# Kernel optimization log

Measured on AMD Instinct MI355X. Metric: run time of the kernel, lower is better.

The kernel has to match this reference:

```python
import jax, jax.numpy as jnp
import numpy as np

N = 50000
E = 640000
R = 8


def setup_inputs() -> dict:
    key = jax.random.key(0)
    ks = jax.random.split(key, 12)
    in_c, hid_c, out_c = 128, 128, 64
    s1 = 1.0 / np.sqrt(in_c)
    s2 = 1.0 / np.sqrt(hid_c)
    s3 = 1.0 / np.sqrt(out_c)
    return {
        "x": jax.random.normal(ks[0], (N, in_c), dtype=jnp.float32),
        "edge_index": jax.random.randint(ks[1], (2, E), 0, N),
        "edge_type": jax.random.randint(ks[2], (E,), 0, R),
        # layer 1: per-relation weights, root weight, bias
        "W1": jax.random.uniform(ks[3], (R, in_c, hid_c), minval=-s1, maxval=s1, dtype=jnp.float32),
        "root1": jax.random.uniform(ks[4], (in_c, hid_c), minval=-s1, maxval=s1, dtype=jnp.float32),
        "b1": jnp.zeros((hid_c,), dtype=jnp.float32),
        # layer 2
        "W2": jax.random.uniform(ks[5], (R, hid_c, out_c), minval=-s2, maxval=s2, dtype=jnp.float32),
        "root2": jax.random.uniform(ks[6], (hid_c, out_c), minval=-s2, maxval=s2, dtype=jnp.float32),
        "b2": jnp.zeros((out_c,), dtype=jnp.float32),
        # classifier
        "Wc": jax.random.uniform(ks[7], (out_c, 2), minval=-s3, maxval=s3, dtype=jnp.float32),
        "bc": jnp.zeros((2,), dtype=jnp.float32),
    }


def _rgcn_layer(x, edge_index, edge_type, W, root, b):
    # PyG RGCNConv with aggr='mean': per relation r, mean-aggregate source
    # features over edges of type r into destinations, then apply W_r.
    # out = sum_r mean_agg_r(x) @ W_r + x @ root + b
    src, dst = edge_index[0], edge_index[1]
    msgs = x[src]  # [E, Fin] gather
    seg = edge_type * N + dst  # combined (relation, dst) segment id
    sums = jax.ops.segment_sum(msgs, seg, num_segments=R * N)  # [R*N, Fin]
    cnt = jax.ops.segment_sum(jnp.ones((msgs.shape[0],), x.dtype), seg, num_segments=R * N)
    mean = sums / jnp.maximum(cnt, 1.0)[:, None]  # zero-degree -> 0
    mean = mean.reshape(R, N, x.shape[1])  # [R, N, Fin]
    out = jnp.einsum("rnf,rfo->no", mean, W) + x @ root + b
    return out


def reference(x, edge_index, edge_type, W1, root1, b1, W2, root2, b2, Wc, bc):
    h = jax.nn.relu(_rgcn_layer(x, edge_index, edge_type, W1, root1, b1))
    # dropout (p=0.3) is identity in eval mode
    h = jax.nn.relu(_rgcn_layer(h, edge_index, edge_type, W2, root2, b2))
    logits = h @ Wc + bc  # [N, 2]
    return logits
```

## Files before the change

### kernel.cpp

```cpp
#include <hip/hip_runtime.h>

#define NN 50000
#define EE 640000
#define RR 8
#define CAP 64

typedef __bf16 bf16x8 __attribute__((ext_vector_type(8)));
typedef float  f32x4  __attribute__((ext_vector_type(4)));
typedef const __attribute__((address_space(1))) unsigned int* gas_p;
typedef __attribute__((address_space(3))) unsigned int* las_p;

__device__ __forceinline__ unsigned short f2b(float f) {
  unsigned int u = __float_as_uint(f);
  u += 0x7fffu + ((u >> 16) & 1u);
  return (unsigned short)(u >> 16);
}
__device__ __forceinline__ float b2f(unsigned short h) {
  return __uint_as_float(((unsigned int)h) << 16);
}

__global__ void k_f32_to_bf16_x4(const float* __restrict__ src,
                                 unsigned short* __restrict__ dst, int n4) {
  int t = blockIdx.x * blockDim.x + threadIdx.x;
  if (t >= n4) return;
  float4 v = reinterpret_cast<const float4*>(src)[t];
  ushort4 o = make_ushort4(f2b(v.x), f2b(v.y), f2b(v.z), f2b(v.w));
  reinterpret_cast<ushort4*>(dst)[t] = o;
}

__global__ void k_build_b1(const float* __restrict__ W1, const float* __restrict__ root1,
                           unsigned short* __restrict__ B1T) {
  int t = blockIdx.x * 256 + threadIdx.x;
  if (t >= 1152 * 128) return;
  int j = t >> 7, k = t & 127;
  float v = (j < 1024) ? W1[((j >> 7) << 14) + (k << 7) + (j & 127)]
                       : root1[(k << 7) + (j - 1024)];
  B1T[t] = f2b(v);
}

__global__ void k_build_b2(const float* __restrict__ W2, const float* __restrict__ root2,
                           unsigned short* __restrict__ B2T) {
  int t = blockIdx.x * 256 + threadIdx.x;
  if (t >= 640 * 128) return;
  int j = t >> 7, k = t & 127;
  float v = 0.0f;
  if (j < 512)      v = W2[((j >> 6) << 13) + (k << 6) + (j & 63)];
  else if (j < 576) v = root2[(k << 6) + (j - 512)];
  B2T[t] = f2b(v);
}

__global__ void k_edges(const int* __restrict__ src, const int* __restrict__ dst,
                        const int* __restrict__ typ,
                        int* __restrict__ cursor, unsigned int* __restrict__ entries) {
  int e = blockIdx.x * 256 + threadIdx.x;
  if (e >= EE) return;
  int d = dst[e], r = typ[e];
  int pos = atomicAdd(&cursor[d], 1);
  if (pos < CAP)
    entries[d * CAP + pos] = (unsigned int)src[e] | ((unsigned int)r << 16);
}

__global__ __launch_bounds__(256, 2) void k_gemm(
    const unsigned short* __restrict__ A, const unsigned short* __restrict__ BT,
    unsigned short* __restrict__ Y, float* __restrict__ rootOut,
    const float* __restrict__ bias, int M, int nsplit, int nroot, int nsub) {
  __shared__ __align__(16) unsigned short As[128 * 128];
  __shared__ __align__(16) unsigned short Bs[2][64 * 128];
  const int tid = threadIdx.x;
  const int m0 = blockIdx.x * 128;
  const int n0g = blockIdx.y * nsub * 64;

  {
#pragma unroll
    for (int c = 0; c < 8; ++c) {
      int L = tid + c * 256;
      int r = L >> 4, c16 = L & 15;
      int j = c16 ^ (r & 15);
      __builtin_amdgcn_global_load_lds(
          (gas_p)(const void*)(A + (size_t)(m0 + r) * 128 + j * 8),
          (las_p)(void*)(As + r * 128 + c16 * 8), 16, 0, 0);
    }
    const unsigned short* Gb = BT + (size_t)n0g * 128;
#pragma unroll
    for (int c = 0; c < 4; ++c) {
      int L = tid + c * 256;
      int r = L >> 4, c16 = L & 15;
      int j = c16 ^ (r & 15);
      __builtin_amdgcn_global_load_lds(
          (gas_p)(const void*)(Gb + (size_t)r * 128 + j * 8),
          (las_p)(void*)(Bs[0] + r * 128 + c16 * 8), 16, 0, 0);
    }
  }
  __syncthreads();

  const int lane = tid & 63;
  const int wave = tid >> 6;
  const int wm = (wave >> 1) << 6;
  const int wn = (wave & 1) << 5;
  const int l15 = lane & 15;
  const int quad = lane >> 4;

  const int tr = lane >> 2;
  const int tc = lane & 3;
  const int sl0 = ((tc & 1) << 1) * 16 + tr;
  const int sl1 = sl0 + 16;
  const bool thi = (tc & 2) != 0;

  int buf = 0;
  for (int s = 0; s < nsub; ++s) {
    if (s + 1 < nsub) {
      const unsigned short* Gb = BT + (size_t)(n0g + (s + 1) * 64) * 128;
      unsigned short* Lb = Bs[buf ^ 1];
#pragma unroll
      for (int c = 0; c < 4; ++c) {
        int L = tid + c * 256;
        int r = L >> 4, c16 = L & 15;
        int j = c16 ^ (r & 15);
        __builtin_amdgcn_global_load_lds(
            (gas_p)(const void*)(Gb + (size_t)r * 128 + j * 8),
            (las_p)(void*)(Lb + r * 128 + c16 * 8), 16, 0, 0);
      }
    }

    f32x4 acc[4][2] = {};
    const unsigned short* Bc = Bs[buf];
#pragma unroll
    for (int kk = 0; kk < 4; ++kk) {
      const int sw = ((kk * 4 + quad) ^ l15) * 8;
      bf16x8 af[4], bfr[2];
#pragma unroll
      for (int i = 0; i < 4; ++i)
        af[i] = *reinterpret_cast<const bf16x8*>(&As[(wm + i * 16 + l15) * 128 + sw]);
#pragma unroll
      for (int j = 0; j < 2; ++j)
        bfr[j] = *reinterpret_cast<const bf16x8*>(&Bc[(wn + j * 16 + l15) * 128 + sw]);
#pragma unroll
      for (int i = 0; i < 4; ++i)
#pragma unroll
        for (int j = 0; j < 2; ++j)
          acc[i][j] = __builtin_amdgcn_mfma_f32_16x16x32_bf16(bfr[j], af[i], acc[i][j], 0, 0, 0);
    }
    __syncthreads();

    const int scol = n0g + s * 64;
    if (scol >= nsplit) {
#pragma unroll
      for (int i = 0; i < 4; ++i) {
        const int m = wm + i * 16 + l15;
        if (m0 + m >= M) continue;
#pragma unroll
        for (int j = 0; j < 2; ++j) {
          const int col = scol + wn + j * 16 + quad * 4 - nsplit;
          if (col < nroot) {
            float4 b4 = *reinterpret_cast<const float4*>(&bias[col]);
            float4 v = make_float4(acc[i][j][0] + b4.x, acc[i][j][1] + b4.y,
                                   acc[i][j][2] + b4.z, acc[i][j][3] + b4.w);
            *reinterpret_cast<float4*>(&rootOut[(size_t)(m0 + m) * nroot + col]) = v;
          }
        }
      }
    } else {
#pragma unroll
      for (int i = 0; i < 4; ++i) {
        uint2 pk0, pk1;
        pk0.x = (unsigned int)f2b(acc[i][0][0]) | ((unsigned int)f2b(acc[i][0][1]) << 16);
        pk0.y = (unsigned int)f2b(acc[i][0][2]) | ((unsigned int)f2b(acc[i][0][3]) << 16);
        pk1.x = (unsigned int)f2b(acc[i][1][0]) | ((unsigned int)f2b(acc[i][1][1]) << 16);
        pk1.y = (unsigned int)f2b(acc[i][1][2]) | ((unsigned int)f2b(acc[i][1][3]) << 16);
        unsigned int a0x = __shfl(pk0.x, sl0, 64), a0y = __shfl(pk0.y, sl0, 64);
        unsigned int a1x = __shfl(pk1.x, sl0, 64), a1y = __shfl(pk1.y, sl0, 64);
        unsigned int b0x = __shfl(pk0.x, sl1, 64), b0y = __shfl(pk0.y, sl1, 64);
        unsigned int b1x = __shfl(pk1.x, sl1, 64), b1y = __shfl(pk1.y, sl1, 64);
        uint4 o;
        o.x = thi ? a1x : a0x;
        o.y = thi ? a1y : a0y;
        o.z = thi ? b1x : b0x;
        o.w = thi ? b1y : b0y;
        const int m = wm + i * 16 + tr;
        if (m0 + m < M)
          *reinterpret_cast<uint4*>(&Y[(size_t)(m0 + m) * nsplit + scol + wn + tc * 8]) = o;
      }
    }
    buf ^= 1;
  }
}

__global__ void k_agg1(const unsigned int* __restrict__ entries,
                       const int* __restrict__ cursor,
                       const unsigned short* __restrict__ y,
                       const float* __restrict__ hpre,
                       unsigned int* __restrict__ hbf) {
  const int d = blockIdx.x * 4 + (threadIdx.x >> 6);
  const int lane = threadIdx.x & 63;
  int deg = cursor[d];
  if (deg > CAP) deg = CAP;
  unsigned int e = (lane < deg) ? entries[d * CAP + lane] : 0u;
  const int myr = (e >> 16) & 7;
  float sc = 0.f;
#pragma unroll
  for (int r = 0; r < 8; ++r) {
    unsigned long long bm = __ballot(lane < deg && myr == r);
    if (myr == r) sc = __builtin_amdgcn_rcpf((float)__popcll(bm));
  }
  if (lane >= deg) sc = 0.f;

  const int g = lane >> 4;
  const int l16 = lane & 15;
  float a[8] = {};
  const int T = (deg + 7) >> 3;
  for (int t = 0; t < T; ++t) {
    const int i0 = t * 8 + g;
    const int i1 = i0 + 4;
    unsigned int e0 = __shfl(e, i0, 64);  float s0 = __shfl(sc, i0, 64);
    unsigned int e1 = __shfl(e, i1, 64);  float s1 = __shfl(sc, i1, 64);
    uint4 pk0 = *reinterpret_cast<const uint4*>(
        y + (((size_t)(e0 & 0xffffu)) << 10) + (((e0 >> 16) & 7u) << 7) + (l16 << 3));
    uint4 pk1 = *reinterpret_cast<const uint4*>(
        y + (((size_t)(e1 & 0xffffu)) << 10) + (((e1 >> 16) & 7u) << 7) + (l16 << 3));
    a[0] += b2f((unsigned short)pk0.x) * s0;
    a[1] += __uint_as_float(pk0.x & 0xffff0000u) * s0;
    a[2] += b2f((unsigned short)pk0.y) * s0;
    a[3] += __uint_as_float(pk0.y & 0xffff0000u) * s0;
    a[4] += b2f((unsigned short)pk0.z) * s0;
    a[5] += __uint_as_float(pk0.z & 0xffff0000u) * s0;
    a[6] += b2f((unsigned short)pk0.w) * s0;
    a[7] += __uint_as_float(pk0.w & 0xffff0000u) * s0;
    a[0] += b2f((unsigned short)pk1.x) * s1;
    a[1] += __uint_as_float(pk1.x & 0xffff0000u) * s1;
    a[2] += b2f((unsigned short)pk1.y) * s1;
    a[3] += __uint_as_float(pk1.y & 0xffff0000u) * s1;
    a[4] += b2f((unsigned short)pk1.z) * s1;
    a[5] += __uint_as_float(pk1.z & 0xffff0000u) * s1;
    a[6] += b2f((unsigned short)pk1.w) * s1;
    a[7] += __uint_as_float(pk1.w & 0xffff0000u) * s1;
  }
#pragma unroll
  for (int j = 0; j < 8; ++j) {
    a[j] += __shfl_xor(a[j], 16, 64);
    a[j] += __shfl_xor(a[j], 32, 64);
  }
  if (g == 0) {
    const float4* hp = reinterpret_cast<const float4*>(hpre) + (size_t)d * 32 + l16 * 2;
    float4 h0 = hp[0];
    float4 h1 = hp[1];
    float v0 = fmaxf(a[0] + h0.x, 0.f), v1 = fmaxf(a[1] + h0.y, 0.f);
    float v2 = fmaxf(a[2] + h0.z, 0.f), v3 = fmaxf(a[3] + h0.w, 0.f);
    float v4 = fmaxf(a[4] + h1.x, 0.f), v5 = fmaxf(a[5] + h1.y, 0.f);
    float v6 = fmaxf(a[6] + h1.z, 0.f), v7 = fmaxf(a[7] + h1.w, 0.f);
    uint4 o;
    o.x = (unsigned int)f2b(v0) | ((unsigned int)f2b(v1) << 16);
    o.y = (unsigned int)f2b(v2) | ((unsigned int)f2b(v3) << 16);
    o.z = (unsigned int)f2b(v4) | ((unsigned int)f2b(v5) << 16);
    o.w = (unsigned int)f2b(v6) | ((unsigned int)f2b(v7) << 16);
    reinterpret_cast<uint4*>(hbf)[(size_t)d * 16 + l16] = o;
  }
}

__global__ void k_agg2(const unsigned int* __restrict__ entries,
                       const int* __restrict__ cursor,
                       const unsigned short* __restrict__ y,
                       const float* __restrict__ hpre,
                       const float* __restrict__ Wc, const float* __restrict__ bc,
                       float* __restrict__ out) {
  const int d = blockIdx.x * 4 + (threadIdx.x >> 6);
  const int lane = threadIdx.x & 63;
  int deg = cursor[d];
  if (deg > CAP) deg = CAP;
  unsigned int e = (lane < deg) ? entries[d * CAP + lane] : 0u;
  const int myr = (e >> 16) & 7;
  float sc = 0.f;
#pragma unroll
  for (int r = 0; r < 8; ++r) {
    unsigned long long bm = __ballot(lane < deg && myr == r);
    if (myr == r) sc = __builtin_amdgcn_rcpf((float)__popcll(bm));
  }
  if (lane >= deg) sc = 0.f;

  const int g = lane >> 3;
  const int l8 = lane & 7;
  float a[8] = {};
  const int T = (deg + 15) >> 4;
  for (int t = 0; t < T; ++t) {
    const int i0 = t * 16 + g;
    const int i1 = i0 + 8;
    unsigned int e0 = __shfl(e, i0, 64);  float s0 = __shfl(sc, i0, 64);
    unsigned int e1 = __shfl(e, i1, 64);  float s1 = __shfl(sc, i1, 64);
    uint4 pk0 = *reinterpret_cast<const uint4*>(
        y + (((size_t)(e0 & 0xffffu)) << 9) + (((e0 >> 16) & 7u) << 6) + (l8 << 3));
    uint4 pk1 = *reinterpret_cast<const uint4*>(
        y + (((size_t)(e1 & 0xffffu)) << 9) + (((e1 >> 16) & 7u) << 6) + (l8 << 3));
    a[0] += b2f((unsigned short)pk0.x) * s0;
    a[1] += __uint_as_float(pk0.x & 0xffff0000u) * s0;
    a[2] += b2f((unsigned short)pk0.y) * s0;
    a[3] += __uint_as_float(pk0.y & 0xffff0000u) * s0;
    a[4] += b2f((unsigned short)pk0.z) * s0;
    a[5] += __uint_as_float(pk0.z & 0xffff0000u) * s0;
    a[6] += b2f((unsigned short)pk0.w) * s0;
    a[7] += __uint_as_float(pk0.w & 0xffff0000u) * s0;
    a[0] += b2f((unsigned short)pk1.x) * s1;
    a[1] += __uint_as_float(pk1.x & 0xffff0000u) * s1;
    a[2] += b2f((unsigned short)pk1.y) * s1;
    a[3] += __uint_as_float(pk1.y & 0xffff0000u) * s1;
    a[4] += b2f((unsigned short)pk1.z) * s1;
    a[5] += __uint_as_float(pk1.z & 0xffff0000u) * s1;
    a[6] += b2f((unsigned short)pk1.w) * s1;
    a[7] += __uint_as_float(pk1.w & 0xffff0000u) * s1;
  }
#pragma unroll
  for (int j = 0; j < 8; ++j) {
    a[j] += __shfl_xor(a[j], 8, 64);
    a[j] += __shfl_xor(a[j], 16, 64);
    a[j] += __shfl_xor(a[j], 32, 64);
  }
  const float4* hp = reinterpret_cast<const float4*>(hpre) + (size_t)d * 16 + l8 * 2;
  float4 h0 = hp[0];
  float4 h1 = hp[1];
  float v0 = fmaxf(a[0] + h0.x, 0.f), v1 = fmaxf(a[1] + h0.y, 0.f);
  float v2 = fmaxf(a[2] + h0.z, 0.f), v3 = fmaxf(a[3] + h0.w, 0.f);
  float v4 = fmaxf(a[4] + h1.x, 0.f), v5 = fmaxf(a[5] + h1.y, 0.f);
  float v6 = fmaxf(a[6] + h1.z, 0.f), v7 = fmaxf(a[7] + h1.w, 0.f);
  const float4* wc4 = reinterpret_cast<const float4*>(Wc) + l8 * 4;
  float4 w0 = wc4[0], w1 = wc4[1], w2 = wc4[2], w3 = wc4[3];
  float p0 = v0 * w0.x + v1 * w0.z + v2 * w1.x + v3 * w1.z
           + v4 * w2.x + v5 * w2.z + v6 * w3.x + v7 * w3.z;
  float p1 = v0 * w0.y + v1 * w0.w + v2 * w1.y + v3 * w1.w
           + v4 * w2.y + v5 * w2.w + v6 * w3.y + v7 * w3.w;
  p0 += __shfl_xor(p0, 1, 64); p1 += __shfl_xor(p1, 1, 64);
  p0 += __shfl_xor(p0, 2, 64); p1 += __shfl_xor(p1, 2, 64);
  p0 += __shfl_xor(p0, 4, 64); p1 += __shfl_xor(p1, 4, 64);
  if (lane == 0) {
    out[d * 2 + 0] = p0 + bc[0];
    out[d * 2 + 1] = p1 + bc[1];
  }
}

extern "C" void kernel_launch(void* const* d_in, const int* in_sizes, int n_in,
                              void* d_out, int out_size, void* d_ws, size_t ws_size,
                              hipStream_t stream) {
  const float* x     = (const float*)d_in[0];
  const int*   ei    = (const int*)d_in[1];
  const int*   et    = (const int*)d_in[2];
  const float* W1    = (const float*)d_in[3];
  const float* root1 = (const float*)d_in[4];
  const float* b1    = (const float*)d_in[5];
  const float* W2    = (const float*)d_in[6];
  const float* root2 = (const float*)d_in[7];
  const float* b2    = (const float*)d_in[8];
  const float* Wc    = (const float*)d_in[9];
  const float* bc    = (const float*)d_in[10];
  const int* srcI = ei;
  const int* dstI = ei + EE;

  char* ws = (char*)d_ws;
  unsigned short* xb      = (unsigned short*)(ws);
  unsigned int*   hbf     = (unsigned int*)(ws);
  unsigned short* B1T     = (unsigned short*)(ws + 12800000);
  unsigned short* B2T     = (unsigned short*)(ws + 13094912);
  int*            cursor  = (int*)(ws + 13258752);
  unsigned int*   entries = (unsigned int*)(ws + 13458752);
  float*          hpre    = (float*)(ws + 26258752);
  unsigned short* y1      = (unsigned short*)(ws + 51858752);
  unsigned short* y2      = y1;

  hipMemsetAsync(cursor, 0, 200000, stream);
  k_f32_to_bf16_x4<<<(1600000 + 255) / 256, 256, 0, stream>>>(x, xb, 1600000);
  k_build_b1<<<(1152 * 128 + 255) / 256, 256, 0, stream>>>(W1, root1, B1T);
  k_build_b2<<<(640 * 128 + 255) / 256, 256, 0, stream>>>(W2, root2, B2T);
  k_edges<<<(EE + 255) / 256, 256, 0, stream>>>(srcI, dstI, et, cursor, entries);

  k_gemm<<<dim3(391, 3), 256, 0, stream>>>(xb, B1T, y1, hpre, b1, NN, 1024, 128, 6);
  k_agg1<<<NN / 4, 256, 0, stream>>>(entries, cursor, y1, hpre, hbf);

  k_gemm<<<dim3(391, 2), 256, 0, stream>>>((const unsigned short*)hbf, B2T, y2, hpre, b2, NN, 512, 64, 5);
  k_agg2<<<NN / 4, 256, 0, stream>>>(entries, cursor, y2, hpre, Wc, bc, (float*)d_out);
}
```

Baseline: 278.5 us.

## Fuse prologue kernels and hold GEMM A-fragments in registers instead of LDS

New measurement: 263.9 us. -5.3%, faster.

```diff
diff --git a/kernel.cpp b/kernel.cpp
--- a/kernel.cpp
+++ b/kernel.cpp
@@ -19,34 +19,41 @@
   return __uint_as_float(((unsigned int)h) << 16);
 }
 
-__global__ void k_f32_to_bf16_x4(const float* __restrict__ src,
-                                 unsigned short* __restrict__ dst, int n4) {
-  int t = blockIdx.x * blockDim.x + threadIdx.x;
-  if (t >= n4) return;
-  float4 v = reinterpret_cast<const float4*>(src)[t];
-  ushort4 o = make_ushort4(f2b(v.x), f2b(v.y), f2b(v.z), f2b(v.w));
-  reinterpret_cast<ushort4*>(dst)[t] = o;
-}
-
-__global__ void k_build_b1(const float* __restrict__ W1, const float* __restrict__ root1,
-                           unsigned short* __restrict__ B1T) {
+#define CONV_N 1600000
+#define B1_N (1152 * 128)
+#define B2_N (640 * 128)
+__global__ void k_prologue(const float* __restrict__ x, unsigned short* __restrict__ xb,
+                           const float* __restrict__ W1, const float* __restrict__ root1,
+                           unsigned short* __restrict__ B1T,
+                           const float* __restrict__ W2, const float* __restrict__ root2,
+                           unsigned short* __restrict__ B2T,
+                           int* __restrict__ cursor) {
   int t = blockIdx.x * 256 + threadIdx.x;
-  if (t >= 1152 * 128) return;
-  int j = t >> 7, k = t & 127;
-  float v = (j < 1024) ? W1[((j >> 7) << 14) + (k << 7) + (j & 127)]
-                       : root1[(k << 7) + (j - 1024)];
-  B1T[t] = f2b(v);
-}
-
-__global__ void k_build_b2(const float* __restrict__ W2, const float* __restrict__ root2,
-                           unsigned short* __restrict__ B2T) {
-  int t = blockIdx.x * 256 + threadIdx.x;
-  if (t >= 640 * 128) return;
-  int j = t >> 7, k = t & 127;
-  float v = 0.0f;
-  if (j < 512)      v = W2[((j >> 6) << 13) + (k << 6) + (j & 63)];
-  else if (j < 576) v = root2[(k << 6) + (j - 512)];
-  B2T[t] = f2b(v);
+  if (t < CONV_N) {
+    float4 v = reinterpret_cast<const float4*>(x)[t];
+    ushort4 o = make_ushort4(f2b(v.x), f2b(v.y), f2b(v.z), f2b(v.w));
+    reinterpret_cast<ushort4*>(xb)[t] = o;
+    return;
+  }
+  t -= CONV_N;
+  if (t < B1_N) {
+    int j = t >> 7, k = t & 127;
+    float v = (j < 1024) ? W1[((j >> 7) << 14) + (k << 7) + (j & 127)]
+                         : root1[(k << 7) + (j - 1024)];
+    B1T[t] = f2b(v);
+    return;
+  }
+  t -= B1_N;
+  if (t < B2_N) {
+    int j = t >> 7, k = t & 127;
+    float v = 0.0f;
+    if (j < 512)      v = W2[((j >> 6) << 13) + (k << 6) + (j & 63)];
+    else if (j < 576) v = root2[(k << 6) + (j - 512)];
+    B2T[t] = f2b(v);
+    return;
+  }
+  t -= B2_N;
+  if (t < NN) cursor[t] = 0;
 }
 
 __global__ void k_edges(const int* __restrict__ src, const int* __restrict__ dst,
@@ -60,26 +67,22 @@
     entries[d * CAP + pos] = (unsigned int)src[e] | ((unsigned int)r << 16);
 }
 
-__global__ __launch_bounds__(256, 2) void k_gemm(
+__global__ __launch_bounds__(256, 3) void k_gemm(
     const unsigned short* __restrict__ A, const unsigned short* __restrict__ BT,
     unsigned short* __restrict__ Y, float* __restrict__ rootOut,
     const float* __restrict__ bias, int M, int nsplit, int nroot, int nsub) {
-  __shared__ __align__(16) unsigned short As[128 * 128];
   __shared__ __align__(16) unsigned short Bs[2][64 * 128];
   const int tid = threadIdx.x;
   const int m0 = blockIdx.x * 128;
   const int n0g = blockIdx.y * nsub * 64;
+  const int lane = tid & 63;
+  const int wave = tid >> 6;
+  const int wm = (wave >> 1) << 6;
+  const int wn = (wave & 1) << 5;
+  const int l15 = lane & 15;
+  const int quad = lane >> 4;
 
   {
-#pragma unroll
-    for (int c = 0; c < 8; ++c) {
-      int L = tid + c * 256;
-      int r = L >> 4, c16 = L & 15;
-      int j = c16 ^ (r & 15);
-      __builtin_amdgcn_global_load_lds(
-          (gas_p)(const void*)(A + (size_t)(m0 + r) * 128 + j * 8),
-          (las_p)(void*)(As + r * 128 + c16 * 8), 16, 0, 0);
-    }
     const unsigned short* Gb = BT + (size_t)n0g * 128;
 #pragma unroll
     for (int c = 0; c < 4; ++c) {
@@ -91,14 +94,16 @@
           (las_p)(void*)(Bs[0] + r * 128 + c16 * 8), 16, 0, 0);
     }
   }
+
+  bf16x8 af[4][4];
+#pragma unroll
+  for (int kk = 0; kk < 4; ++kk)
+#pragma unroll
+    for (int i = 0; i < 4; ++i)
+      af[kk][i] = *reinterpret_cast<const bf16x8*>(
+          A + (size_t)(m0 + wm + i * 16 + l15) * 128 + (kk * 4 + quad) * 8);
+
   __syncthreads();
-
-  const int lane = tid & 63;
-  const int wave = tid >> 6;
-  const int wm = (wave >> 1) << 6;
-  const int wn = (wave & 1) << 5;
-  const int l15 = lane & 15;
-  const int quad = lane >> 4;
 
   const int tr = lane >> 2;
   const int tc = lane & 3;
@@ -127,10 +132,7 @@
 #pragma unroll
     for (int kk = 0; kk < 4; ++kk) {
       const int sw = ((kk * 4 + quad) ^ l15) * 8;
-      bf16x8 af[4], bfr[2];
-#pragma unroll
-      for (int i = 0; i < 4; ++i)
-        af[i] = *reinterpret_cast<const bf16x8*>(&As[(wm + i * 16 + l15) * 128 + sw]);
+      bf16x8 bfr[2];
 #pragma unroll
       for (int j = 0; j < 2; ++j)
         bfr[j] = *reinterpret_cast<const bf16x8*>(&Bc[(wn + j * 16 + l15) * 128 + sw]);
@@ -138,7 +140,7 @@
       for (int i = 0; i < 4; ++i)
 #pragma unroll
         for (int j = 0; j < 2; ++j)
-          acc[i][j] = __builtin_amdgcn_mfma_f32_16x16x32_bf16(bfr[j], af[i], acc[i][j], 0, 0, 0);
+          acc[i][j] = __builtin_amdgcn_mfma_f32_16x16x32_bf16(bfr[j], af[kk][i], acc[i][j], 0, 0, 0);
     }
     __syncthreads();
 
@@ -362,10 +364,9 @@
   unsigned short* y1      = (unsigned short*)(ws + 51858752);
   unsigned short* y2      = y1;
 
-  hipMemsetAsync(cursor, 0, 200000, stream);
-  k_f32_to_bf16_x4<<<(1600000 + 255) / 256, 256, 0, stream>>>(x, xb, 1600000);
-  k_build_b1<<<(1152 * 128 + 255) / 256, 256, 0, stream>>>(W1, root1, B1T);
-  k_build_b2<<<(640 * 128 + 255) / 256, 256, 0, stream>>>(W2, root2, B2T);
+  const int PRO_N = CONV_N + B1_N + B2_N + NN;
+  k_prologue<<<(PRO_N + 255) / 256, 256, 0, stream>>>(x, xb, W1, root1, B1T,
+                                                      W2, root2, B2T, cursor);
   k_edges<<<(EE + 255) / 256, 256, 0, stream>>>(srcI, dstI, et, cursor, entries);
 
   k_gemm<<<dim3(391, 3), 256, 0, stream>>>(xb, B1T, y1, hpre, b1, NN, 1024, 128, 6);
```
